# Kernel optimization log

Hardware: AMD Instinct MI355X
Metric: run time of the kernel (lower is better)

The kernel has to match this reference:

```python
import jax, jax.numpy as jnp
import numpy as np

N_NODES = 100000
N_EDGES = 1600000


def _sage_conv(x, src, dst, W_l, W_r, b):
    """PyG SAGEConv (mean aggr): lin_l(mean of neighbor feats) + b + lin_r(x)."""
    n = x.shape[0]
    msgs = x[src]                                            # [E, F] gather
    agg = jax.ops.segment_sum(msgs, dst, num_segments=n)     # [N, F]
    cnt = jax.ops.segment_sum(jnp.ones((src.shape[0],), x.dtype), dst,
                              num_segments=n)                # [N]
    mean = agg / jnp.maximum(cnt, 1.0)[:, None]
    return mean @ W_l + b + x @ W_r


def setup_inputs() -> dict:
    key = jax.random.key(0)
    ks = jax.random.split(key, 8)
    x = jax.random.normal(ks[0], (N_NODES, 64), dtype=jnp.float32)
    edge_index = jax.random.randint(ks[1], (2, N_EDGES), 0, N_NODES, dtype=jnp.int64)
    # Glorot-ish small init for weights
    W1_l = jax.random.normal(ks[2], (64, 128), dtype=jnp.float32) * 0.1
    W1_r = jax.random.normal(ks[3], (64, 128), dtype=jnp.float32) * 0.1
    b1 = jax.random.normal(ks[4], (128,), dtype=jnp.float32) * 0.1
    W2_l = jax.random.normal(ks[5], (128, 64), dtype=jnp.float32) * 0.1
    W2_r = jax.random.normal(ks[6], (128, 64), dtype=jnp.float32) * 0.1
    b2 = jax.random.normal(ks[7], (64,), dtype=jnp.float32) * 0.1
    return {"x": x, "edge_index": edge_index, "W1_l": W1_l, "W1_r": W1_r,
            "b1": b1, "W2_l": W2_l, "W2_r": W2_r, "b2": b2}


def reference(x, edge_index, W1_l, W1_r, b1, W2_l, W2_r, b2):
    src, dst = edge_index[0], edge_index[1]
    h = jax.nn.relu(_sage_conv(x, src, dst, W1_l, W1_r, b1))  # [N, 128]
    out = _sage_conv(h, src, dst, W2_l, W2_r, b2)             # [N, 64]
    return out
```

## Files before the change

kernel.cpp:

```cpp
#include <hip/hip_runtime.h>
#include <hip/hip_bf16.h>
#include <stdint.h>


typedef unsigned short u16;
typedef __attribute__((ext_vector_type(8))) short short8;
typedef __attribute__((ext_vector_type(4))) float f32x4;

#define BSHIFT 9
#define BSIZE  512
#define CHUNK  8192
#define NCP    256

__device__ __forceinline__ float bf2f(u16 v) { return __uint_as_float(((uint32_t)v) << 16); }
__device__ __forceinline__ float bfu_lo(uint32_t u) { return __uint_as_float(u << 16); }
__device__ __forceinline__ float bfu_hi(uint32_t u) { return __uint_as_float(u & 0xffff0000u); }
__device__ __forceinline__ u16 f2bf(float f) {
    uint32_t u = __float_as_uint(f);
    return (u16)((u + 0x7fffu + ((u >> 16) & 1u)) >> 16);
}

__device__ __forceinline__ int wave_scan(int v) {
    int lane = threadIdx.x & 63;
#pragma unroll
    for (int d = 1; d < 64; d <<= 1) {
        int t = __shfl_up(v, d);
        if (lane >= d) v += t;
    }
    return v;
}

__device__ __forceinline__ int block_scan512(int v, int* ws, int* ptot) {
    int tid = threadIdx.x, lane = tid & 63, wid = tid >> 6;
    int s = wave_scan(v);
    if (lane == 63) ws[wid] = s;
    __syncthreads();
    int add = 0, tot = 0;
#pragma unroll
    for (int w = 0; w < 8; w++) { int x = ws[w]; tot += x; if (w < wid) add += x; }
    if (ptot) *ptot = tot;
    __syncthreads();
    return s + add;
}

__device__ __forceinline__ int block_scan256(int v, int* ws, int* ptot) {
    int tid = threadIdx.x, lane = tid & 63, wid = tid >> 6;
    int s = wave_scan(v);
    if (lane == 63) ws[wid] = s;
    __syncthreads();
    int add = 0, tot = 0;
#pragma unroll
    for (int w = 0; w < 4; w++) { int x = ws[w]; tot += x; if (w < wid) add += x; }
    if (ptot) *ptot = tot;
    __syncthreads();
    return s + add;
}

__global__ __launch_bounds__(512) void setup_k(
    const void* __restrict__ x, const void* __restrict__ ei,
    const void* __restrict__ W1l, const void* __restrict__ W1r,
    const void* __restrict__ b1, const void* __restrict__ W2l,
    const void* __restrict__ W2r, const void* __restrict__ b2,
    u16* __restrict__ wpk, u16* __restrict__ xb,
    int* __restrict__ hist2d, int* __restrict__ flags,
    int nn, int ne, int nb, int nchunk, int ncvt,
    int c0, int c1, int c2, int c3, int c4, int c5, int c6) {
    __shared__ int sh[512];
    __shared__ int sflag;
    int bid = blockIdx.x, tid = threadIdx.x;
    if (bid < nchunk) {
        sh[tid] = 0;
        int samp = 0;
        if (tid < 32) {
            long long n32 = 2LL * ne;
            long long stride = n32 / 32; if (stride < 1) stride = 1;
            long long i = (long long)tid * stride; i |= 1;
            if (i >= n32) i = 1;
            samp = (((const int*)ei)[i] != 0);
        }
        unsigned long long m = __ballot(samp);
        if (tid == 0) sflag = (m == 0ULL) ? 1 : 0;
        __syncthreads();
        int e64 = sflag;
        int base = bid * CHUNK;
#pragma unroll
        for (int j = 0; j < 16; j++) {
            int e = base + j * 512 + tid;
            if (e < ne) {
                int dst = e64 ? (int)((const long long*)ei)[(size_t)ne + e]
                              : ((const int*)ei)[(size_t)ne + e];
                if ((unsigned)dst < (unsigned)nn) atomicAdd(&sh[dst >> BSHIFT], 1);
            }
        }
        __syncthreads();
        for (int b = tid; b < nb; b += 512)
            hist2d[b * NCP + bid] = sh[b];
    } else if (bid < nchunk + ncvt) {
        int samp = 0;
        if (tid < 32) {
            int C = c0; int stride = C / 32; if (stride < 1) stride = 1;
            long long i = (long long)tid * stride;
            if (i > C - 1) i = C - 1; i &= ~1LL;
            u16 v = ((const u16*)x)[i];
            int e = (v >> 7) & 0xFF;
            samp = ((e >= 0x50 && e <= 0x97) || v == 0) ? 1 : 0;
        }
        unsigned long long m = __ballot(samp);
        if (tid == 0) sflag = (__popcll(m) >= 24) ? 1 : 0;
        __syncthreads();
        if (sflag) return;
        int i = (bid - nchunk) * 512 + tid;
        if (i < nn * 16) {
            float4 f = ((const float4*)x)[i];
            *(ushort4*)&xb[(size_t)i * 4] =
                make_ushort4(f2bf(f.x), f2bf(f.y), f2bf(f.z), f2bf(f.w));
        }
    } else if (bid < nchunk + ncvt + 4) {
        int b = bid - nchunk - ncvt;
        const void* src = (b == 0) ? W1l : (b == 1) ? W1r : (b == 2) ? W2l : W2r;
        int C = (b == 0) ? c1 : (b == 1) ? c2 : (b == 2) ? c4 : c5;
        int samp = 0;
        if (tid < 32) {
            int stride = C / 32; if (stride < 1) stride = 1;
            long long i = (long long)tid * stride;
            if (i > C - 1) i = C - 1; i &= ~1LL;
            u16 v = ((const u16*)src)[i];
            int e = (v >> 7) & 0xFF;
            samp = ((e >= 0x50 && e <= 0x97) || v == 0) ? 1 : 0;
        }
        unsigned long long m = __ballot(samp);
        if (tid == 0) sflag = (__popcll(m) >= 24) ? 1 : 0;
        __syncthreads();
        int isbf = sflag;
        u16* dst = wpk + ((b >= 2) ? (16384 + (b - 2) * 8192) : 0);
        for (int i = tid; i < 2048; i += 512) {
            u16 v0, v1, v2, v3;
            if (isbf) {
                ushort4 u = ((const ushort4*)src)[i];
                v0 = u.x; v1 = u.y; v2 = u.z; v3 = u.w;
            } else {
                float4 u = ((const float4*)src)[i];
                v0 = f2bf(u.x); v1 = f2bf(u.y); v2 = f2bf(u.z); v3 = f2bf(u.w);
            }
            int k, n, k8;
            if (b <= 1) { k = i >> 5; n = (i & 31) * 4; k8 = (b == 1 ? 8 : 0) + (k >> 3); }
            else        { k = i >> 4; n = (i & 15) * 4; k8 = k >> 3; }
            int kc = k8 >> 2, q = k8 & 3, w = k & 7;
            int basei = ((n >> 4) * 4 + kc) * 512 + (q * 16 + (n & 15)) * 8 + w;
            dst[basei] = v0; dst[basei + 8] = v1; dst[basei + 16] = v2; dst[basei + 24] = v3;
        }
    } else {
        int a = tid >> 5, lane = tid & 31;
        if (tid < 8) sh[tid] = 0;
        __syncthreads();
        if (a < 7) {
            const void* ptrs[7] = {x, W1l, W1r, b1, W2l, W2r, b2};
            int cs[7] = {c0, c1, c2, c3, c4, c5, c6};
            int C = cs[a];
            int stride = C / 32; if (stride < 1) stride = 1;
            long long i = (long long)lane * stride;
            if (i > C - 1) i = C - 1;
            i &= ~1LL;
            u16 v = ((const u16*)ptrs[a])[i];
            int e = (v >> 7) & 0xFF;
            int sane = ((e >= 0x50 && e <= 0x97) || v == 0) ? 1 : 0;
            atomicAdd(&sh[a], sane);
        } else if (a == 7) {
            long long n32 = 2LL * ne;
            long long stride = n32 / 32; if (stride < 1) stride = 1;
            long long i = (long long)lane * stride; i |= 1;
            if (i >= n32) i = 1;
            int wv = ((const int*)ei)[i];
            atomicAdd(&sh[7], wv != 0 ? 1 : 0);
        }
        __syncthreads();
        if (tid < 7) flags[tid] = (sh[tid] >= 24) ? 1 : 0;
        if (tid == 7) flags[7] = (sh[7] == 0) ? 1 : 0;
    }
}

__global__ __launch_bounds__(256) void scan2d(
    const int* __restrict__ hist2d, int* __restrict__ base2d,
    int* __restrict__ btot, int nchunk) {
    __shared__ int ws[4];
    int b = blockIdx.x, tid = threadIdx.x;
    int v = (tid < nchunk) ? hist2d[b * NCP + tid] : 0;
    int tot;
    int inc = block_scan256(v, ws, &tot);
    if (tid < nchunk) base2d[b * NCP + tid] = inc - v;
    if (tid == 0) btot[b] = tot;
}

__global__ __launch_bounds__(512) void partition_k(
    const void* __restrict__ ei, const int* __restrict__ btot,
    const int* __restrict__ base2d,
    unsigned* __restrict__ ep, int nn, int ne, int nb) {
    __shared__ unsigned stage[CHUNK];
    __shared__ u16 ab[CHUNK];
    __shared__ int hist[512], exl[512], gbase[512], lcur[512];
    __shared__ int ws[8];
    __shared__ int e64s;
    int tid = threadIdx.x;
    int base = blockIdx.x * CHUNK;
    hist[tid] = 0;
    int samp = 0;
    if (tid < 32) {
        long long n32 = 2LL * ne;
        long long stride = n32 / 32; if (stride < 1) stride = 1;
        long long i = (long long)tid * stride; i |= 1;
        if (i >= n32) i = 1;
        samp = (((const int*)ei)[i] != 0);
    }
    unsigned long long bm = __ballot(samp);
    if (tid == 0) e64s = (bm == 0ULL) ? 1 : 0;
    __syncthreads();
    int e64 = e64s;
    unsigned pk[16]; int bk[16];
#pragma unroll
    for (int j = 0; j < 16; j++) {
        int e = base + j * 512 + tid;
        bk[j] = -1;
        pk[j] = 0;
        if (e < ne) {
            int src, dst;
            if (e64) {
                src = (int)((const long long*)ei)[e];
                dst = (int)((const long long*)ei)[(size_t)ne + e];
            } else {
                src = ((const int*)ei)[e];
                dst = ((const int*)ei)[(size_t)ne + e];
            }
            if ((unsigned)dst < (unsigned)nn) {
                if ((unsigned)src >= (unsigned)nn) src = 0;
                bk[j] = dst >> BSHIFT;
                pk[j] = (unsigned)src | ((unsigned)(dst & (BSIZE - 1)) << 17);
                atomicAdd(&hist[bk[j]], 1);
            }
        }
    }
    __syncthreads();
    int hv = hist[tid];
    int tot;
    int inc1 = block_scan512(hv, ws, &tot);
    int ex = inc1 - hv;
    exl[tid] = ex;
    lcur[tid] = ex;
    int bv = (tid < nb) ? btot[tid] : 0;
    int inc2 = block_scan512(bv, ws, nullptr);
    int bo_t = inc2 - bv;
    gbase[tid] = (tid < nb) ? (bo_t + base2d[tid * NCP + blockIdx.x]) : 0;
    __syncthreads();
#pragma unroll
    for (int j = 0; j < 16; j++) {
        if (bk[j] >= 0) {
            int r = atomicAdd(&lcur[bk[j]], 1);
            stage[r] = pk[j];
            ab[r] = (u16)bk[j];
        }
    }
    __syncthreads();
    for (int j = tid; j < tot; j += 512) {
        int b = ab[j];
        ep[gbase[b] + (j - exl[b])] = stage[j];
    }
}

__global__ __launch_bounds__(512) void csr_fill2(
    const unsigned* __restrict__ ep, const int* __restrict__ btot,
    int* __restrict__ off, int* __restrict__ cnt, int* __restrict__ esrc,
    int nn, int nb) {
    __shared__ int hist[BSIZE], lcur[BSIZE];
    __shared__ int ws[8];
    __shared__ int s_end;
    int b = blockIdx.x;
    int tid = threadIdx.x;
    int bv = (tid < nb) ? btot[tid] : 0;
    int incb = block_scan512(bv, ws, nullptr);
    if (tid == b) s_end = incb;
    hist[tid] = 0;
    __syncthreads();
    int end = s_end;
    int beg = end - btot[b];
    for (int j = beg + tid; j < end; j += 512)
        atomicAdd(&hist[(ep[j] >> 17) & (BSIZE - 1)], 1);
    __syncthreads();
    int hv = hist[tid];
    int inc = block_scan512(hv, ws, nullptr);
    int ex = beg + inc - hv;
    lcur[tid] = ex;
    int node = b * BSIZE + tid;
    if (node < nn) { off[node] = ex; cnt[node] = hv; }
    __syncthreads();
    for (int j = beg + tid; j < end; j += 512) {
        unsigned p = ep[j];
        int r = atomicAdd(&lcur[(p >> 17) & (BSIZE - 1)], 1);
        esrc[r] = (int)(p & 0x1FFFFu);
    }
}

__global__ __launch_bounds__(512, 8) void layer1(
    const void* __restrict__ x, const u16* __restrict__ xb,
    const int* __restrict__ esrc,
    const int* __restrict__ off, const int* __restrict__ cnt,
    const u16* __restrict__ w1g, const u16* __restrict__ w2lg,
    const u16* __restrict__ w2rg, const void* __restrict__ b1,
    u16* __restrict__ g, u16* __restrict__ rr,
    const int* __restrict__ flags, int nn) {
    __shared__ __align__(16) u16 wA[8 * 512];
    __shared__ float b_s[128];
    int tid = threadIdx.x;
    int node0 = blockIdx.x * 32;

    if (tid < 128) b_s[tid] = flags[3] ? bf2f(((const u16*)b1)[tid]) : ((const float*)b1)[tid];

    int grp = tid >> 4, gl = tid & 15;
    int n = node0 + grp;
    int mtile = grp >> 4, l15m = grp & 15;
    int idx_mean = (mtile * 4 + (gl >> 3)) * 512 + (((gl >> 1) & 3) * 16 + l15m) * 8 + (gl & 1) * 4;
    int idx_x = (mtile * 4 + 2 + (gl >> 3)) * 512 + (((gl >> 1) & 3) * 16 + l15m) * 8 + (gl & 1) * 4;
    const u16* xs = flags[0] ? (const u16*)x : xb;
    if (n < nn) {
        int beg = off[n], deg = cnt[n];
        float a0 = 0.f, a1 = 0.f, a2 = 0.f, a3 = 0.f;
        int i = 0;
        const u16* xbp = xs + gl * 4;
        for (; i + 16 <= deg; i += 16) {
            ushort4 v[16];
#pragma unroll
            for (int j = 0; j < 16; j++) {
                int s0 = esrc[beg + i + j];
                v[j] = *(const ushort4*)(xbp + (size_t)s0 * 64);
            }
#pragma unroll
            for (int j = 0; j < 16; j++) {
                a0 += bf2f(v[j].x); a1 += bf2f(v[j].y);
                a2 += bf2f(v[j].z); a3 += bf2f(v[j].w);
            }
        }
        for (; i + 8 <= deg; i += 8) {
            ushort4 v[8];
#pragma unroll
            for (int j = 0; j < 8; j++) {
                int s0 = esrc[beg + i + j];
                v[j] = *(const ushort4*)(xbp + (size_t)s0 * 64);
            }
#pragma unroll
            for (int j = 0; j < 8; j++) {
                a0 += bf2f(v[j].x); a1 += bf2f(v[j].y);
                a2 += bf2f(v[j].z); a3 += bf2f(v[j].w);
            }
        }
        for (; i < deg; i++) {
            int s0 = esrc[beg + i];
            ushort4 v = *(const ushort4*)(xbp + (size_t)s0 * 64);
            a0 += bf2f(v.x); a1 += bf2f(v.y); a2 += bf2f(v.z); a3 += bf2f(v.w);
        }
        float inv = 1.0f / (float)(deg > 0 ? deg : 1);
        *(ushort4*)&wA[idx_mean] =
            make_ushort4(f2bf(a0 * inv), f2bf(a1 * inv), f2bf(a2 * inv), f2bf(a3 * inv));
        *(ushort4*)&wA[idx_x] = *(const ushort4*)(xs + (size_t)n * 64 + gl * 4);
    } else {
        *(ushort4*)&wA[idx_mean] = make_ushort4(0, 0, 0, 0);
        *(ushort4*)&wA[idx_x] = make_ushort4(0, 0, 0, 0);
    }
    __syncthreads();

    int wv = tid >> 6, lane = tid & 63;
    int l15 = lane & 15, q = lane >> 4;
    f32x4 acc0 = {0.f, 0.f, 0.f, 0.f};
    f32x4 acc1 = {0.f, 0.f, 0.f, 0.f};
#pragma unroll
    for (int kc = 0; kc < 4; kc++) {
        short8 a0 = *(const short8*)&wA[(kc) * 512 + lane * 8];
        short8 a1 = *(const short8*)&wA[(4 + kc) * 512 + lane * 8];
        short8 b  = *(const short8*)&w1g[(wv * 4 + kc) * 512 + lane * 8];
        acc0 = __builtin_amdgcn_mfma_f32_16x16x32_bf16(a0, b, acc0, 0, 0, 0);
        acc1 = __builtin_amdgcn_mfma_f32_16x16x32_bf16(a1, b, acc1, 0, 0, 0);
    }
    int nc = wv * 16 + l15;
    float bias = b_s[nc];
    u16 hv0[4], hv1[4];
#pragma unroll
    for (int r = 0; r < 4; r++) {
        hv0[r] = f2bf(fmaxf(acc0[r] + bias, 0.0f));
        hv1[r] = f2bf(fmaxf(acc1[r] + bias, 0.0f));
    }
    __syncthreads();
    int kcg = wv >> 1;
    int qg  = ((wv & 1) << 1) | (l15 >> 3);
    int wg  = l15 & 7;
#pragma unroll
    for (int r = 0; r < 4; r++) {
        int m = q * 4 + r;
        wA[kcg * 512 + (qg * 16 + m) * 8 + wg]       = hv0[r];
        wA[(4 + kcg) * 512 + (qg * 16 + m) * 8 + wg] = hv1[r];
    }
    __syncthreads();
    int mt2 = wv >> 2, nt2 = wv & 3;
    f32x4 ag = {0.f, 0.f, 0.f, 0.f};
    f32x4 ar = {0.f, 0.f, 0.f, 0.f};
#pragma unroll
    for (int kc = 0; kc < 4; kc++) {
        short8 a = *(const short8*)&wA[(mt2 * 4 + kc) * 512 + lane * 8];
        short8 bl = *(const short8*)&w2lg[(nt2 * 4 + kc) * 512 + lane * 8];
        short8 br = *(const short8*)&w2rg[(nt2 * 4 + kc) * 512 + lane * 8];
        ag = __builtin_amdgcn_mfma_f32_16x16x32_bf16(a, bl, ag, 0, 0, 0);
        ar = __builtin_amdgcn_mfma_f32_16x16x32_bf16(a, br, ar, 0, 0, 0);
    }
    __syncthreads();
    int nc2 = nt2 * 16 + l15;
#pragma unroll
    for (int r = 0; r < 4; r++) {
        int m = mt2 * 16 + q * 4 + r;
        wA[m * 64 + nc2]        = f2bf(ag[r]);
        wA[2048 + m * 64 + nc2] = f2bf(ar[r]);
    }
    __syncthreads();
    int half = tid >> 8, idx = tid & 255;
    int row = idx >> 3, seg = idx & 7;
    int nd = node0 + row;
    if (nd < nn) {
        uint4 v = *(const uint4*)&wA[half * 2048 + row * 64 + seg * 8];
        u16* dst = (half ? rr : g) + (size_t)nd * 64 + seg * 8;
        *(uint4*)dst = v;
    }
}

__global__ __launch_bounds__(512, 8) void layer2(
    const u16* __restrict__ g, const u16* __restrict__ rr,
    const int* __restrict__ esrc,
    const int* __restrict__ off, const int* __restrict__ cnt,
    const void* __restrict__ b2, void* __restrict__ out,
    const int* __restrict__ flags, int nn) {
    __shared__ float b_s[64];
    int tid = threadIdx.x;
    int node0 = blockIdx.x * 32;
    int obf = flags[0];
    if (tid < 64) b_s[tid] = flags[6] ? bf2f(((const u16*)b2)[tid]) : ((const float*)b2)[tid];
    __syncthreads();

    int grp = tid >> 4, gl = tid & 15;
    int n = node0 + grp;
    if (n >= nn) return;
    int beg = off[n], deg = cnt[n];
    float a0 = 0.f, a1 = 0.f, a2 = 0.f, a3 = 0.f;
    const u16* gb = g + gl * 4;
    int i = 0;
    for (; i + 16 <= deg; i += 16) {
        uint2 v[16];
#pragma unroll
        for (int j = 0; j < 16; j++) {
            int s0 = esrc[beg + i + j];
            v[j] = *(const uint2*)(gb + (size_t)s0 * 64);
        }
#pragma unroll
        for (int j = 0; j < 16; j++) {
            a0 += bfu_lo(v[j].x); a1 += bfu_hi(v[j].x);
            a2 += bfu_lo(v[j].y); a3 += bfu_hi(v[j].y);
        }
    }
    for (; i + 8 <= deg; i += 8) {
        uint2 v[8];
#pragma unroll
        for (int j = 0; j < 8; j++) {
            int s0 = esrc[beg + i + j];
            v[j] = *(const uint2*)(gb + (size_t)s0 * 64);
        }
#pragma unroll
        for (int j = 0; j < 8; j++) {
            a0 += bfu_lo(v[j].x); a1 += bfu_hi(v[j].x);
            a2 += bfu_lo(v[j].y); a3 += bfu_hi(v[j].y);
        }
    }
    for (; i < deg; i++) {
        int s0 = esrc[beg + i];
        uint2 v = *(const uint2*)(gb + (size_t)s0 * 64);
        a0 += bfu_lo(v.x); a1 += bfu_hi(v.x);
        a2 += bfu_lo(v.y); a3 += bfu_hi(v.y);
    }
    float inv = 1.0f / (float)(deg > 0 ? deg : 1);
    uint2 rv = *(const uint2*)(rr + (size_t)n * 64 + gl * 4);
    float o0 = a0 * inv + bfu_lo(rv.x) + b_s[gl * 4 + 0];
    float o1 = a1 * inv + bfu_hi(rv.x) + b_s[gl * 4 + 1];
    float o2 = a2 * inv + bfu_lo(rv.y) + b_s[gl * 4 + 2];
    float o3 = a3 * inv + bfu_hi(rv.y) + b_s[gl * 4 + 3];
    if (obf) {
        u16* op = (u16*)out + (size_t)n * 64 + gl * 4;
        *(ushort4*)op = make_ushort4(f2bf(o0), f2bf(o1), f2bf(o2), f2bf(o3));
    } else {
        float* op = (float*)out + (size_t)n * 64 + gl * 4;
        *(float4*)op = make_float4(o0, o1, o2, o3);
    }
}

__global__ __launch_bounds__(256) void zero_out_k(u16* __restrict__ out, int n) {
    int i = blockIdx.x * 256 + threadIdx.x;
    if (i < n) out[i] = 0;
}

extern "C" void kernel_launch(void* const* d_in, const int* in_sizes, int n_in,
                              void* d_out, int out_size, void* d_ws, size_t ws_size,
                              hipStream_t stream) {
    const void* x   = d_in[0];
    const void* ei  = d_in[1];
    const void* W1l = d_in[2];
    const void* W1r = d_in[3];
    const void* b1  = d_in[4];
    const void* W2l = d_in[5];
    const void* W2r = d_in[6];
    const void* b2  = d_in[7];

    int nn = in_sizes[0] / 64;
    int ne = in_sizes[1] / 2;
    int nb = (nn + BSIZE - 1) / BSIZE;
    int nchunk = (ne + CHUNK - 1) / CHUNK;

    auto al = [](size_t v) { return (v + 255) & ~(size_t)255; };
    size_t o_flags = 0;
    size_t o_btot  = 256;
    size_t o_wpk   = al(o_btot + 512 * 4);
    size_t o_cnt   = al(o_wpk + 65536);
    size_t o_off   = al(o_cnt + (size_t)nn * 4);
    size_t o_esrc  = al(o_off + (size_t)nn * 4);
    size_t o_r     = al(o_esrc + (size_t)ne * 4);
    size_t o_xb    = al(o_r + (size_t)nn * 64 * 2);
    size_t o_g     = al(o_xb + (size_t)nn * 64 * 2);
    size_t ws_req  = o_g + (size_t)nn * 64 * 2;

    size_t o_ep   = o_r;
    size_t o_h2d  = al(o_ep + (size_t)ne * 4);
    size_t o_b2d  = al(o_h2d + (size_t)512 * NCP * 4);
    size_t ov_end = o_b2d + (size_t)512 * NCP * 4;

    bool ok = ws_size >= ws_req && nb >= 1 && nb <= 512 && nn <= 131072 &&
              nchunk <= NCP && ov_end <= o_xb;
    if (!ok) {
        zero_out_k<<<(out_size + 255) / 256, 256, 0, stream>>>((u16*)d_out, out_size);
        return;
    }

    char* ws = (char*)d_ws;
    int* flags  = (int*)(ws + o_flags);
    int* btot   = (int*)(ws + o_btot);
    u16* wpk    = (u16*)(ws + o_wpk);
    int* cnt    = (int*)(ws + o_cnt);
    int* off    = (int*)(ws + o_off);
    int* esrc   = (int*)(ws + o_esrc);
    u16* rbuf   = (u16*)(ws + o_r);
    u16* xb     = (u16*)(ws + o_xb);
    u16* gbuf   = (u16*)(ws + o_g);
    unsigned* ep = (unsigned*)(ws + o_ep);
    int* hist2d = (int*)(ws + o_h2d);
    int* base2d = (int*)(ws + o_b2d);

    int ncvt = (nn * 16 + 511) / 512;
    setup_k<<<nchunk + ncvt + 5, 512, 0, stream>>>(
        x, ei, W1l, W1r, b1, W2l, W2r, b2, wpk, xb, hist2d, flags,
        nn, ne, nb, nchunk, ncvt,
        in_sizes[0], in_sizes[2], in_sizes[3], in_sizes[4],
        in_sizes[5], in_sizes[6], in_sizes[7]);
    scan2d<<<nb, 256, 0, stream>>>(hist2d, base2d, btot, nchunk);
    partition_k<<<nchunk, 512, 0, stream>>>(ei, btot, base2d, ep, nn, ne, nb);
    csr_fill2<<<nb, 512, 0, stream>>>(ep, btot, off, cnt, esrc, nn, nb);
    int lb = (nn + 31) / 32;
    layer1<<<lb, 512, 0, stream>>>(x, xb, esrc, off, cnt,
                                   wpk, wpk + 16384, wpk + 24576, b1,
                                   gbuf, rbuf, flags, nn);
    layer2<<<lb, 512, 0, stream>>>(gbuf, rbuf, esrc, off, cnt, b2, d_out, flags, nn);
}
```

Baseline: 220.9 us.

## Drop scan2d kernel; recompute bucket prefix sums inside partition and CSR fill

Removes the separate scan2d launch, which turned the per-chunk bucket histogram into per-bucket totals and exclusive offsets. Each partition_k and csr_fill2 block now reads the histogram column for its buckets across all chunks and sums it directly. The histogram is transposed to chunk-major layout so those reads coalesce across threads. This saves one kernel launch and its dependency gap, but every block now does redundant reads of the whole histogram (about 196 chunks times 196 buckets).

After: 257.4 us. 16.5% more time.

```diff
diff --git a/kernel.cpp b/kernel.cpp
--- a/kernel.cpp
+++ b/kernel.cpp
@@ -10,7 +10,8 @@
 #define BSHIFT 9
 #define BSIZE  512
 #define CHUNK  8192
-#define NCP    256
+#define NBP    512
+#define NCMAX  256
 
 __device__ __forceinline__ float bf2f(u16 v) { return __uint_as_float(((uint32_t)v) << 16); }
 __device__ __forceinline__ float bfu_lo(uint32_t u) { return __uint_as_float(u << 16); }
@@ -38,19 +39,6 @@
     int add = 0, tot = 0;
 #pragma unroll
     for (int w = 0; w < 8; w++) { int x = ws[w]; tot += x; if (w < wid) add += x; }
-    if (ptot) *ptot = tot;
-    __syncthreads();
-    return s + add;
-}
-
-__device__ __forceinline__ int block_scan256(int v, int* ws, int* ptot) {
-    int tid = threadIdx.x, lane = tid & 63, wid = tid >> 6;
-    int s = wave_scan(v);
-    if (lane == 63) ws[wid] = s;
-    __syncthreads();
-    int add = 0, tot = 0;
-#pragma unroll
-    for (int w = 0; w < 4; w++) { int x = ws[w]; tot += x; if (w < wid) add += x; }
     if (ptot) *ptot = tot;
     __syncthreads();
     return s + add;
@@ -93,8 +81,7 @@
             }
         }
         __syncthreads();
-        for (int b = tid; b < nb; b += 512)
-            hist2d[b * NCP + bid] = sh[b];
+        if (tid < NBP) hist2d[bid * NBP + tid] = (tid < nb) ? sh[tid] : 0;
     } else if (bid < nchunk + ncvt) {
         int samp = 0;
         if (tid < 32) {
@@ -179,22 +166,9 @@
     }
 }
 
-__global__ __launch_bounds__(256) void scan2d(
-    const int* __restrict__ hist2d, int* __restrict__ base2d,
-    int* __restrict__ btot, int nchunk) {
-    __shared__ int ws[4];
-    int b = blockIdx.x, tid = threadIdx.x;
-    int v = (tid < nchunk) ? hist2d[b * NCP + tid] : 0;
-    int tot;
-    int inc = block_scan256(v, ws, &tot);
-    if (tid < nchunk) base2d[b * NCP + tid] = inc - v;
-    if (tid == 0) btot[b] = tot;
-}
-
 __global__ __launch_bounds__(512) void partition_k(
-    const void* __restrict__ ei, const int* __restrict__ btot,
-    const int* __restrict__ base2d,
-    unsigned* __restrict__ ep, int nn, int ne, int nb) {
+    const void* __restrict__ ei, const int* __restrict__ hist2d,
+    unsigned* __restrict__ ep, int nn, int ne, int nb, int nchunk) {
     __shared__ unsigned stage[CHUNK];
     __shared__ u16 ab[CHUNK];
     __shared__ int hist[512], exl[512], gbase[512], lcur[512];
@@ -245,10 +219,18 @@
     int ex = inc1 - hv;
     exl[tid] = ex;
     lcur[tid] = ex;
-    int bv = (tid < nb) ? btot[tid] : 0;
-    int inc2 = block_scan512(bv, ws, nullptr);
-    int bo_t = inc2 - bv;
-    gbase[tid] = (tid < nb) ? (bo_t + base2d[tid * NCP + blockIdx.x]) : 0;
+    int baseb = 0, tbt = 0;
+    int mybid = blockIdx.x;
+    if (tid < nb) {
+        for (int c = 0; c < nchunk; c++) {
+            int h = hist2d[c * NBP + tid];
+            tbt += h;
+            if (c < mybid) baseb += h;
+        }
+    }
+    int inc2 = block_scan512(tbt, ws, nullptr);
+    int bo_t = inc2 - tbt;
+    gbase[tid] = (tid < nb) ? (bo_t + baseb) : 0;
     __syncthreads();
 #pragma unroll
     for (int j = 0; j < 16; j++) {
@@ -266,21 +248,24 @@
 }
 
 __global__ __launch_bounds__(512) void csr_fill2(
-    const unsigned* __restrict__ ep, const int* __restrict__ btot,
+    const unsigned* __restrict__ ep, const int* __restrict__ hist2d,
     int* __restrict__ off, int* __restrict__ cnt, int* __restrict__ esrc,
-    int nn, int nb) {
+    int nn, int nb, int nchunk) {
     __shared__ int hist[BSIZE], lcur[BSIZE];
     __shared__ int ws[8];
-    __shared__ int s_end;
+    __shared__ int s_end, s_cnt;
     int b = blockIdx.x;
     int tid = threadIdx.x;
-    int bv = (tid < nb) ? btot[tid] : 0;
-    int incb = block_scan512(bv, ws, nullptr);
-    if (tid == b) s_end = incb;
+    int tbt = 0;
+    if (tid < nb) {
+        for (int c = 0; c < nchunk; c++) tbt += hist2d[c * NBP + tid];
+    }
+    int incb = block_scan512(tbt, ws, nullptr);
+    if (tid == b) { s_end = incb; s_cnt = tbt; }
     hist[tid] = 0;
     __syncthreads();
     int end = s_end;
-    int beg = end - btot[b];
+    int beg = end - s_cnt;
     for (int j = beg + tid; j < end; j += 512)
         atomicAdd(&hist[(ep[j] >> 17) & (BSIZE - 1)], 1);
     __syncthreads();
@@ -517,8 +502,7 @@
 
     auto al = [](size_t v) { return (v + 255) & ~(size_t)255; };
     size_t o_flags = 0;
-    size_t o_btot  = 256;
-    size_t o_wpk   = al(o_btot + 512 * 4);
+    size_t o_wpk   = 256;
     size_t o_cnt   = al(o_wpk + 65536);
     size_t o_off   = al(o_cnt + (size_t)nn * 4);
     size_t o_esrc  = al(o_off + (size_t)nn * 4);
@@ -529,11 +513,10 @@
 
     size_t o_ep   = o_r;
     size_t o_h2d  = al(o_ep + (size_t)ne * 4);
-    size_t o_b2d  = al(o_h2d + (size_t)512 * NCP * 4);
-    size_t ov_end = o_b2d + (size_t)512 * NCP * 4;
+    size_t ov_end = o_h2d + (size_t)NCMAX * NBP * 4;
 
     bool ok = ws_size >= ws_req && nb >= 1 && nb <= 512 && nn <= 131072 &&
-              nchunk <= NCP && ov_end <= o_xb;
+              nchunk <= NCMAX && ov_end <= o_xb;
     if (!ok) {
         zero_out_k<<<(out_size + 255) / 256, 256, 0, stream>>>((u16*)d_out, out_size);
         return;
@@ -541,7 +524,6 @@
 
     char* ws = (char*)d_ws;
     int* flags  = (int*)(ws + o_flags);
-    int* btot   = (int*)(ws + o_btot);
     u16* wpk    = (u16*)(ws + o_wpk);
     int* cnt    = (int*)(ws + o_cnt);
     int* off    = (int*)(ws + o_off);
@@ -551,7 +533,6 @@
     u16* gbuf   = (u16*)(ws + o_g);
     unsigned* ep = (unsigned*)(ws + o_ep);
     int* hist2d = (int*)(ws + o_h2d);
-    int* base2d = (int*)(ws + o_b2d);
 
     int ncvt = (nn * 16 + 511) / 512;
     setup_k<<<nchunk + ncvt + 5, 512, 0, stream>>>(
@@ -559,9 +540,8 @@
         nn, ne, nb, nchunk, ncvt,
         in_sizes[0], in_sizes[2], in_sizes[3], in_sizes[4],
         in_sizes[5], in_sizes[6], in_sizes[7]);
-    scan2d<<<nb, 256, 0, stream>>>(hist2d, base2d, btot, nchunk);
-    partition_k<<<nchunk, 512, 0, stream>>>(ei, btot, base2d, ep, nn, ne, nb);
-    csr_fill2<<<nb, 512, 0, stream>>>(ep, btot, off, cnt, esrc, nn, nb);
+    partition_k<<<nchunk, 512, 0, stream>>>(ei, hist2d, ep, nn, ne, nb, nchunk);
+    csr_fill2<<<nb, 512, 0, stream>>>(ep, hist2d, off, cnt, esrc, nn, nb, nchunk);
     int lb = (nn + 31) / 32;
     layer1<<<lb, 512, 0, stream>>>(x, xb, esrc, off, cnt,
                                    wpk, wpk + 16384, wpk + 24576, b1,
```

## Fuse CSR build stages into one cooperative kernel with grid syncs

Applied to the files above, without the earlier changes.

Merges the histogram, per-bucket scan, partition and CSR-fill stages into a single cooperative kernel of 256 blocks that uses grid.sync between phases, replacing four separate launches. The remaining setup kernel then only does conversion and weight packing. This targets launch gaps and tail idle time between the small graph-building kernels. The cost is fewer resident blocks (grid-stride loops over chunks and buckets) and grid-wide barriers. If the cooperative launch fails, the old multi-kernel path runs instead.

Result: slower. 332.8 us (+50.7%).

```diff
diff --git a/kernel.cpp b/kernel.cpp
--- a/kernel.cpp
+++ b/kernel.cpp
@@ -1,7 +1,10 @@
 #include <hip/hip_runtime.h>
 #include <hip/hip_bf16.h>
+#include <hip/hip_cooperative_groups.h>
 #include <stdint.h>
 
+
+namespace cg = cooperative_groups;
 
 typedef unsigned short u16;
 typedef __attribute__((ext_vector_type(8))) short short8;
@@ -43,17 +46,145 @@
     return s + add;
 }
 
-__device__ __forceinline__ int block_scan256(int v, int* ws, int* ptot) {
-    int tid = threadIdx.x, lane = tid & 63, wid = tid >> 6;
-    int s = wave_scan(v);
-    if (lane == 63) ws[wid] = s;
-    __syncthreads();
-    int add = 0, tot = 0;
-#pragma unroll
-    for (int w = 0; w < 4; w++) { int x = ws[w]; tot += x; if (w < wid) add += x; }
-    if (ptot) *ptot = tot;
-    __syncthreads();
-    return s + add;
+__global__ __launch_bounds__(512) void build_k(
+    const void* __restrict__ ei, int* __restrict__ hist2d,
+    int* __restrict__ base2d, int* __restrict__ btot,
+    unsigned* __restrict__ ep, int* __restrict__ off,
+    int* __restrict__ cnt, int* __restrict__ esrc,
+    int nn, int ne, int nb, int nchunk) {
+    cg::grid_group grid = cg::this_grid();
+    __shared__ unsigned stage[CHUNK];
+    __shared__ u16 ab[CHUNK];
+    __shared__ int hist[512], exl[512], gbase[512], lcur[512];
+    __shared__ int ws[8];
+    __shared__ int e64s, s_end;
+    int tid = threadIdx.x;
+    int G = gridDim.x;
+
+    int samp = 0;
+    if (tid < 32) {
+        long long n32 = 2LL * ne;
+        long long stride = n32 / 32; if (stride < 1) stride = 1;
+        long long i = (long long)tid * stride; i |= 1;
+        if (i >= n32) i = 1;
+        samp = (((const int*)ei)[i] != 0);
+    }
+    unsigned long long bm = __ballot(samp);
+    if (tid == 0) e64s = (bm == 0ULL) ? 1 : 0;
+    __syncthreads();
+    int e64 = e64s;
+
+    for (int c = blockIdx.x; c < nchunk; c += G) {
+        hist[tid] = 0;
+        __syncthreads();
+        int base = c * CHUNK;
+#pragma unroll
+        for (int j = 0; j < 16; j++) {
+            int e = base + j * 512 + tid;
+            if (e < ne) {
+                int dst = e64 ? (int)((const long long*)ei)[(size_t)ne + e]
+                              : ((const int*)ei)[(size_t)ne + e];
+                if ((unsigned)dst < (unsigned)nn) atomicAdd(&hist[dst >> BSHIFT], 1);
+            }
+        }
+        __syncthreads();
+        for (int b = tid; b < nb; b += 512)
+            hist2d[b * NCP + c] = hist[b];
+        __syncthreads();
+    }
+    grid.sync();
+
+    for (int b = blockIdx.x; b < nb; b += G) {
+        int v = (tid < nchunk) ? hist2d[b * NCP + tid] : 0;
+        int tot;
+        int inc = block_scan512(v, ws, &tot);
+        if (tid < nchunk) base2d[b * NCP + tid] = inc - v;
+        if (tid == 0) btot[b] = tot;
+        __syncthreads();
+    }
+    grid.sync();
+
+    for (int c = blockIdx.x; c < nchunk; c += G) {
+        int base = c * CHUNK;
+        hist[tid] = 0;
+        __syncthreads();
+        unsigned pk[16]; int bk[16];
+#pragma unroll
+        for (int j = 0; j < 16; j++) {
+            int e = base + j * 512 + tid;
+            bk[j] = -1;
+            pk[j] = 0;
+            if (e < ne) {
+                int src, dst;
+                if (e64) {
+                    src = (int)((const long long*)ei)[e];
+                    dst = (int)((const long long*)ei)[(size_t)ne + e];
+                } else {
+                    src = ((const int*)ei)[e];
+                    dst = ((const int*)ei)[(size_t)ne + e];
+                }
+                if ((unsigned)dst < (unsigned)nn) {
+                    if ((unsigned)src >= (unsigned)nn) src = 0;
+                    bk[j] = dst >> BSHIFT;
+                    pk[j] = (unsigned)src | ((unsigned)(dst & (BSIZE - 1)) << 17);
+                    atomicAdd(&hist[bk[j]], 1);
+                }
+            }
+        }
+        __syncthreads();
+        int hv = hist[tid];
+        int tot;
+        int inc1 = block_scan512(hv, ws, &tot);
+        int ex = inc1 - hv;
+        exl[tid] = ex;
+        lcur[tid] = ex;
+        int bv = (tid < nb) ? btot[tid] : 0;
+        int inc2 = block_scan512(bv, ws, nullptr);
+        int bo_t = inc2 - bv;
+        gbase[tid] = (tid < nb) ? (bo_t + base2d[tid * NCP + c]) : 0;
+        __syncthreads();
+#pragma unroll
+        for (int j = 0; j < 16; j++) {
+            if (bk[j] >= 0) {
+                int r = atomicAdd(&lcur[bk[j]], 1);
+                stage[r] = pk[j];
+                ab[r] = (u16)bk[j];
+            }
+        }
+        __syncthreads();
+        for (int j = tid; j < tot; j += 512) {
+            int b = ab[j];
+            ep[gbase[b] + (j - exl[b])] = stage[j];
+        }
+        __syncthreads();
+    }
+    grid.sync();
+
+    for (int b = blockIdx.x; b < nb; b += G) {
+        int bv = (tid < nb) ? btot[tid] : 0;
+        int incb = block_scan512(bv, ws, nullptr);
+        if (tid == b) s_end = incb;
+        hist[tid] = 0;
+        __syncthreads();
+        int end = s_end;
+        int beg = end - btot[b];
+        for (int j = beg + tid; j < end; j += 512)
+            atomicAdd(&hist[(ep[j] >> 17) & (BSIZE - 1)], 1);
+        __syncthreads();
+        int hv = hist[tid];
+        int inc = block_scan512(hv, ws, nullptr);
+        int ex = beg + inc - hv;
+        lcur[tid] = ex;
+        int node = b * BSIZE + tid;
+        if (node < nn) { off[node] = ex; cnt[node] = hv; }
+        __syncthreads();
+        for (int j = beg + tid; j < end; j += 512) {
+            unsigned p = ep[j];
+            int r = atomicAdd(&lcur[(p >> 17) & (BSIZE - 1)], 1);
+            esrc[r] = (int)(p & 0x1FFFFu);
+        }
+        __syncthreads();
+    }
 }
 
 __global__ __launch_bounds__(512) void setup_k(
@@ -179,14 +310,14 @@
     }
 }
 
-__global__ __launch_bounds__(256) void scan2d(
+__global__ __launch_bounds__(512) void scan2d(
     const int* __restrict__ hist2d, int* __restrict__ base2d,
     int* __restrict__ btot, int nchunk) {
-    __shared__ int ws[4];
+    __shared__ int ws[8];
     int b = blockIdx.x, tid = threadIdx.x;
     int v = (tid < nchunk) ? hist2d[b * NCP + tid] : 0;
     int tot;
-    int inc = block_scan256(v, ws, &tot);
+    int inc = block_scan512(v, ws, &tot);
     if (tid < nchunk) base2d[b * NCP + tid] = inc - v;
     if (tid == 0) btot[b] = tot;
 }
@@ -554,14 +685,33 @@
     int* base2d = (int*)(ws + o_b2d);
 
     int ncvt = (nn * 16 + 511) / 512;
-    setup_k<<<nchunk + ncvt + 5, 512, 0, stream>>>(
-        x, ei, W1l, W1r, b1, W2l, W2r, b2, wpk, xb, hist2d, flags,
-        nn, ne, nb, nchunk, ncvt,
-        in_sizes[0], in_sizes[2], in_sizes[3], in_sizes[4],
-        in_sizes[5], in_sizes[6], in_sizes[7]);
-    scan2d<<<nb, 256, 0, stream>>>(hist2d, base2d, btot, nchunk);
-    partition_k<<<nchunk, 512, 0, stream>>>(ei, btot, base2d, ep, nn, ne, nb);
-    csr_fill2<<<nb, 512, 0, stream>>>(ep, btot, off, cnt, esrc, nn, nb);
+
+    const void* a_ei = ei; int* a_h2d = hist2d; int* a_b2d = base2d;
+    int* a_btot = btot; unsigned* a_ep = ep; int* a_off = off;
+    int* a_cnt = cnt; int* a_esrc = esrc;
+    int a_nn = nn, a_ne = ne, a_nb = nb, a_nchunk = nchunk;
+    void* cargs[] = {&a_ei, &a_h2d, &a_b2d, &a_btot, &a_ep, &a_off,
+                     &a_cnt, &a_esrc, &a_nn, &a_ne, &a_nb, &a_nchunk};
+    hipError_t cerr = hipLaunchCooperativeKernel(
+        (const void*)build_k, dim3(256), dim3(512), cargs, 0, stream);
+
+    if (cerr == hipSuccess) {
+        setup_k<<<ncvt + 5, 512, 0, stream>>>(
+            x, ei, W1l, W1r, b1, W2l, W2r, b2, wpk, xb, hist2d, flags,
+            nn, ne, nb, 0, ncvt,
+            in_sizes[0], in_sizes[2], in_sizes[3], in_sizes[4],
+            in_sizes[5], in_sizes[6], in_sizes[7]);
+    } else {
+        setup_k<<<nchunk + ncvt + 5, 512, 0, stream>>>(
+            x, ei, W1l, W1r, b1, W2l, W2r, b2, wpk, xb, hist2d, flags,
+            nn, ne, nb, nchunk, ncvt,
+            in_sizes[0], in_sizes[2], in_sizes[3], in_sizes[4],
+            in_sizes[5], in_sizes[6], in_sizes[7]);
+        scan2d<<<nb, 512, 0, stream>>>(hist2d, base2d, btot, nchunk);
+        partition_k<<<nchunk, 512, 0, stream>>>(ei, btot, base2d, ep, nn, ne, nb);
+        csr_fill2<<<nb, 512, 0, stream>>>(ep, btot, off, cnt, esrc, nn, nb);
+    }
+
     int lb = (nn + 31) / 32;
     layer1<<<lb, 512, 0, stream>>>(x, xb, esrc, off, cnt,
                                    wpk, wpk + 16384, wpk + 24576, b1,
```
